# Kernel optimization log

Hardware: AMD Instinct MI355X
Metric: run time of the kernel (lower is better)

Reference implementation:

```python
import jax, jax.numpy as jnp
import numpy as np

B, T, H = 4, 2048, 1024
NH = 16
DK = H // NH  # 64
EPS = 1e-12


def setup_inputs() -> dict:
    key = jax.random.key(0)
    ks = jax.random.split(key, 20)
    s = 0.02
    inp = {
        "hidden_states": jax.random.normal(ks[0], (B, T, H), jnp.float32),
        "source_states": jax.random.normal(ks[1], (B, T, H), jnp.float32),
        "source_len": jax.random.randint(ks[2], (B,), 0, T, jnp.int64),
        # attention params (Linear: y = x @ W + b)
        "Wq": s * jax.random.normal(ks[3], (H, H), jnp.float32),
        "bq": jnp.zeros((H,), jnp.float32),
        "Wk": s * jax.random.normal(ks[4], (H, H), jnp.float32),
        "bk": jnp.zeros((H,), jnp.float32),
        "Wv": s * jax.random.normal(ks[5], (H, H), jnp.float32),
        "bv": jnp.zeros((H,), jnp.float32),
        "Wd": s * jax.random.normal(ks[6], (H, H), jnp.float32),
        "bd": jnp.zeros((H,), jnp.float32),
        # Fp: Linear -> ReLU -> (dropout, eval=id) -> Linear -> (dropout)
        "Wp1": s * jax.random.normal(ks[7], (H, H), jnp.float32),
        "bp1": jnp.zeros((H,), jnp.float32),
        "Wp2": s * jax.random.normal(ks[8], (H, H), jnp.float32),
        "bp2": jnp.zeros((H,), jnp.float32),
        # LayerNorm
        "ln_g": jnp.ones((H,), jnp.float32),
        "ln_b": jnp.zeros((H,), jnp.float32),
    }
    return inp


def _split_heads(x):
    # (B, T, H) -> (B, NH, T, DK)
    return x.reshape(B, T, NH, DK).transpose(0, 2, 1, 3)


def reference(hidden_states, source_states, source_len, Wq, bq, Wk, bk, Wv, bv,
              Wd, bd, Wp1, bp1, Wp2, bp2, ln_g, ln_b):
    # P = Fp(source_states), masked to valid source positions
    P = jax.nn.relu(source_states @ Wp1 + bp1) @ Wp2 + bp2  # (B,T,H)
    rng = jnp.arange(T)[None, :]                              # (1,T)
    source_mask = rng < source_len[:, None]                   # (B,T) bool
    P = P * source_mask[:, :, None].astype(P.dtype)

    q = _split_heads(hidden_states @ Wq + bq)  # (B,NH,T,DK)
    k = _split_heads(P @ Wk + bk)
    v = _split_heads(P @ Wv + bv)

    scores = jnp.einsum('bhqd,bhkd->bhqk', q, k) / jnp.sqrt(jnp.float32(DK))
    scores = scores + (1.0 - source_mask[:, None, None, :].astype(scores.dtype)) * -10000.0
    probs = jax.nn.softmax(scores.astype(jnp.float32), axis=-1).astype(hidden_states.dtype)

    ctx = jnp.einsum('bhqk,bhkd->bhqd', probs, v)            # (B,NH,T,DK)
    ctx = ctx.transpose(0, 2, 1, 3).reshape(B, T, H)

    attn_out = ctx @ Wd + bd
    x = attn_out + hidden_states
    mu = jnp.mean(x, axis=-1, keepdims=True)
    var = jnp.mean(jnp.square(x - mu), axis=-1, keepdims=True)
    out = (x - mu) * jax.lax.rsqrt(var + EPS) * ln_g + ln_b
    return out
```

## Files before the change

kernel.cpp:

```cpp
#include <hip/hip_runtime.h>
#include <hip/hip_bf16.h>

#define BB 4
#define TT 2048
#define HH 1024
#define NHH 16
#define DKK 64

typedef __attribute__((ext_vector_type(8))) short bf16x8;
typedef __attribute__((ext_vector_type(4))) float f32x4;

__device__ __forceinline__ unsigned short f2bf(float f) {
    union { float f; unsigned u; } v; v.f = f;
    unsigned r = v.u + 0x7fffu + ((v.u >> 16) & 1u);
    return (unsigned short)(r >> 16);
}

__device__ __forceinline__ void gload_lds16(const unsigned short* g, unsigned short* l) {
    __builtin_amdgcn_global_load_lds(
        (const __attribute__((address_space(1))) unsigned int*)g,
        (__attribute__((address_space(3))) unsigned int*)l, 16, 0, 0);
}

__global__ __launch_bounds__(256) void cvt2_kernel(const float* __restrict__ in0,
                                                   const float* __restrict__ in1,
                                                   unsigned short* __restrict__ out0,
                                                   unsigned short* __restrict__ out1, int n4) {
    const float* in = blockIdx.y ? in1 : in0;
    unsigned short* out = blockIdx.y ? out1 : out0;
    int i = blockIdx.x * blockDim.x + threadIdx.x;
    if (i < n4) {
        float4 v = reinterpret_cast<const float4*>(in)[i];
        union { unsigned short u[4]; unsigned long long ll; } o;
        o.u[0] = f2bf(v.x); o.u[1] = f2bf(v.y); o.u[2] = f2bf(v.z); o.u[3] = f2bf(v.w);
        reinterpret_cast<unsigned long long*>(out)[i] = o.ll;
    }
}

__global__ __launch_bounds__(256) void wtcvt6_kernel(
    const float* __restrict__ W0, const float* __restrict__ W1, const float* __restrict__ W2,
    const float* __restrict__ W3, const float* __restrict__ W4, const float* __restrict__ W5,
    unsigned short* __restrict__ T0, unsigned short* __restrict__ T1, unsigned short* __restrict__ T2,
    unsigned short* __restrict__ T3, unsigned short* __restrict__ T4, unsigned short* __restrict__ T5) {
    const float* W; unsigned short* Wt;
    switch (blockIdx.z) {
        case 0: W = W0; Wt = T0; break;
        case 1: W = W1; Wt = T1; break;
        case 2: W = W2; Wt = T2; break;
        case 3: W = W3; Wt = T3; break;
        case 4: W = W4; Wt = T4; break;
        default: W = W5; Wt = T5; break;
    }
    __shared__ float t[32][33];
    int bx = blockIdx.x * 32, by = blockIdx.y * 32;
    int tx = threadIdx.x, ty = threadIdx.y;
#pragma unroll
    for (int i = 0; i < 32; i += 8)
        t[ty + i][tx] = W[(size_t)(by + ty + i) * HH + bx + tx];
    __syncthreads();
#pragma unroll
    for (int i = 0; i < 32; i += 8)
        Wt[(size_t)(bx + ty + i) * HH + by + tx] = f2bf(t[tx][ty + i]);
}

template <int EPI, bool SKIP>
__global__ __launch_bounds__(256) void gemm_kernel(
    const unsigned short* __restrict__ A, const unsigned short* __restrict__ Bt,
    const float* __restrict__ bias, unsigned short* __restrict__ Cb,
    float* __restrict__ Cf, const float* __restrict__ resid,
    const int* __restrict__ slen, int M, int N, int K) {
    __shared__ unsigned short As[128 * 64];
    __shared__ unsigned short Bs[128 * 64];
    int flat = blockIdx.y * 8 + blockIdx.x;
    int xcd = flat & 7, idx = flat >> 3;
    int bx = (idx & 7) * 128;
    int by = (xcd + ((idx >> 3) << 3)) * 128;
    if constexpr (SKIP) {
        int slb = slen[by >> 11];
        int ktend = ((slb + 63) >> 6) << 6;
        if (ktend == 0) ktend = 64;
        if ((by & (TT - 1)) >= ktend) return;
    }
    int tid = threadIdx.x, lane = tid & 63, w = tid >> 6;
    int wr = (w >> 1) * 64, wc = (w & 1) * 64;

    f32x4 acc[4][4] = {};
    for (int k0 = 0; k0 < K; k0 += 64) {
        __syncthreads();
#pragma unroll
        for (int c = 0; c < 4; c++) {
            int idx2 = c * 256 + tid;
            int r = idx2 >> 3, col = (idx2 & 7) * 8;
            gload_lds16(&A[(size_t)(by + r) * K + k0 + col], &As[idx2 * 8]);
            gload_lds16(&Bt[(size_t)(bx + r) * K + k0 + col], &Bs[idx2 * 8]);
        }
        __syncthreads();
#pragma unroll
        for (int kk = 0; kk < 2; kk++) {
            bf16x8 a[4], b[4];
#pragma unroll
            for (int i = 0; i < 4; i++)
                a[i] = *(bf16x8*)&As[(wr + i * 16 + (lane & 15)) * 64 + kk * 32 + (lane >> 4) * 8];
#pragma unroll
            for (int j = 0; j < 4; j++)
                b[j] = *(bf16x8*)&Bs[(wc + j * 16 + (lane & 15)) * 64 + kk * 32 + (lane >> 4) * 8];
#pragma unroll
            for (int i = 0; i < 4; i++)
#pragma unroll
                for (int j = 0; j < 4; j++)
                    acc[i][j] = __builtin_amdgcn_mfma_f32_16x16x32_bf16(a[i], b[j], acc[i][j], 0, 0, 0);
        }
    }

    int sl = 0;
    if constexpr (EPI == 2) sl = slen[by >> 11];
#pragma unroll
    for (int i = 0; i < 4; i++)
#pragma unroll
        for (int j = 0; j < 4; j++)
#pragma unroll
            for (int r = 0; r < 4; r++) {
                int row = by + wr + i * 16 + (lane >> 4) * 4 + r;
                int col = bx + wc + j * 16 + (lane & 15);
                float v = acc[i][j][r] + bias[col];
                if constexpr (EPI == 1) v = fmaxf(v, 0.f);
                if constexpr (EPI == 2) { int t = row & (TT - 1); if (t >= sl) v = 0.f; }
                if constexpr (EPI == 6) v *= 0.18033688f;
                if constexpr (EPI == 1 || EPI == 2) {
                    Cb[(size_t)row * N + col] = f2bf(v);
                } else if constexpr (EPI == 3 || EPI == 6) {
                    int b = row >> 11, t = row & (TT - 1), h = col >> 6, d = col & 63;
                    Cb[((size_t)((b * NHH + h) * TT + t)) * DKK + d] = f2bf(v);
                } else if constexpr (EPI == 4) {
                    int b = row >> 11, t = row & (TT - 1), h = col >> 6, d = col & 63;
                    Cb[((size_t)((b * NHH + h) * DKK + d)) * TT + t] = f2bf(v);
                } else if constexpr (EPI == 5) {
                    Cf[(size_t)row * N + col] = v + resid[(size_t)row * N + col];
                }
            }
}

__global__ __launch_bounds__(512) void attn_kernel(
    const unsigned short* __restrict__ Q, const unsigned short* __restrict__ K,
    const unsigned short* __restrict__ Vt, const int* __restrict__ slen,
    unsigned short* __restrict__ ctx) {
    __shared__ unsigned short Ks[2][64 * 64];
    __shared__ unsigned short Vs[2][64 * 64];
    __shared__ unsigned short Pl[8][16 * 64];
    int tid = threadIdx.x, lane = tid & 63, w = tid >> 6;
    int c = lane & 15, g = lane >> 4;
    int b = blockIdx.z, h = blockIdx.y, q0 = blockIdx.x * 128;
    size_t bh = (size_t)(b * NHH + h);
    int sl = slen[b];
    int ktend = ((sl + 63) >> 6) << 6;
    if (ktend == 0) ktend = 64;

    bf16x8 qf[2];
    int qrow = q0 + w * 16 + c;
#pragma unroll
    for (int half = 0; half < 2; half++)
        qf[half] = *(const bf16x8*)&Q[(bh * TT + qrow) * DKK + half * 32 + g * 8];

    char* Pw = (char*)&Pl[w][0];
    unsigned swz = (unsigned)((c & 7) << 4);

    int sr = tid >> 3, ss = tid & 7;
    int scol = (ss ^ (sr & 7)) * 8;

    gload_lds16(&K[(bh * TT + sr) * DKK + scol], &Ks[0][tid * 8]);
    gload_lds16(&Vt[(bh * DKK + sr) * TT + scol], &Vs[0][tid * 8]);
    int cur = 0;

    float m_ = -INFINITY, l_ = 0.f;
    f32x4 o[4] = {};

    for (int kt = 0; kt < ktend; kt += 64) {
        __syncthreads();
        if (kt + 64 < ktend) {
            gload_lds16(&K[(bh * TT + kt + 64 + sr) * DKK + scol], &Ks[cur ^ 1][tid * 8]);
            gload_lds16(&Vt[(bh * DKK + sr) * TT + kt + 64 + scol], &Vs[cur ^ 1][tid * 8]);
        }

        f32x4 s[4] = {};
        __builtin_amdgcn_s_setprio(1);
#pragma unroll
        for (int j = 0; j < 4; j++)
#pragma unroll
            for (int half = 0; half < 2; half++) {
                bf16x8 kf = *(bf16x8*)((char*)&Ks[cur][0] + (j * 16 + c) * 128 +
                                       (((unsigned)(half * 64 + g * 16)) ^ swz));
                s[j] = __builtin_amdgcn_mfma_f32_16x16x32_bf16(kf, qf[half], s[j], 0, 0, 0);
            }
        __builtin_amdgcn_s_setprio(0);

        if (kt + 64 > sl) {
#pragma unroll
            for (int j = 0; j < 4; j++) {
                int kbase = kt + j * 16 + g * 4;
#pragma unroll
                for (int r = 0; r < 4; r++)
                    if (kbase + r >= sl) s[j][r] = -14427.0f;
            }
        }

        float tmax = -INFINITY;
#pragma unroll
        for (int j = 0; j < 4; j++)
#pragma unroll
            for (int r = 0; r < 4; r++) tmax = fmaxf(tmax, s[j][r]);
        tmax = fmaxf(tmax, __shfl_xor(tmax, 16));
        tmax = fmaxf(tmax, __shfl_xor(tmax, 32));

        float p[4][4];
        float ps = 0.f;
        if (__all(tmax <= m_ + 8.f)) {
#pragma unroll
            for (int j = 0; j < 4; j++)
#pragma unroll
                for (int r = 0; r < 4; r++) {
                    p[j][r] = __builtin_amdgcn_exp2f(s[j][r] - m_);
                    ps += p[j][r];
                }
            ps += __shfl_xor(ps, 16);
            ps += __shfl_xor(ps, 32);
            l_ += ps;
        } else {
            float mn = fmaxf(m_, tmax);
            float alpha = __builtin_amdgcn_exp2f(m_ - mn);
#pragma unroll
            for (int j = 0; j < 4; j++)
#pragma unroll
                for (int r = 0; r < 4; r++) {
                    p[j][r] = __builtin_amdgcn_exp2f(s[j][r] - mn);
                    ps += p[j][r];
                }
            ps += __shfl_xor(ps, 16);
            ps += __shfl_xor(ps, 32);
            l_ = l_ * alpha + ps;
            m_ = mn;
            float av[4];
#pragma unroll
            for (int r = 0; r < 4; r++) av[r] = __shfl(alpha, g * 4 + r);
#pragma unroll
            for (int go = 0; go < 4; go++)
#pragma unroll
                for (int r = 0; r < 4; r++) o[go][r] *= av[r];
        }

#pragma unroll
        for (int j = 0; j < 4; j++) {
            __hip_bfloat162 lo = __float22bfloat162_rn(make_float2(p[j][0], p[j][1]));
            __hip_bfloat162 hi = __float22bfloat162_rn(make_float2(p[j][2], p[j][3]));
            uint2 u;
            u.x = *(unsigned*)&lo;
            u.y = *(unsigned*)&hi;
            *(uint2*)(Pw + c * 128 + (((unsigned)(j * 32 + g * 8)) ^ swz)) = u;
        }
        bf16x8 pf0 = *(bf16x8*)(Pw + c * 128 + (((unsigned)(g * 16)) ^ swz));
        bf16x8 pf1 = *(bf16x8*)(Pw + c * 128 + (((unsigned)(64 + g * 16)) ^ swz));

        __builtin_amdgcn_s_setprio(1);
#pragma unroll
        for (int go = 0; go < 4; go++) {
            bf16x8 vf0 = *(bf16x8*)((char*)&Vs[cur][0] + (go * 16 + c) * 128 +
                                    (((unsigned)(g * 16)) ^ swz));
            o[go] = __builtin_amdgcn_mfma_f32_16x16x32_bf16(pf0, vf0, o[go], 0, 0, 0);
            bf16x8 vf1 = *(bf16x8*)((char*)&Vs[cur][0] + (go * 16 + c) * 128 +
                                    (((unsigned)(64 + g * 16)) ^ swz));
            o[go] = __builtin_amdgcn_mfma_f32_16x16x32_bf16(pf1, vf1, o[go], 0, 0, 0);
        }
        __builtin_amdgcn_s_setprio(0);
        cur ^= 1;
    }

    float linv[4];
#pragma unroll
    for (int r = 0; r < 4; r++) linv[r] = 1.f / __shfl(l_, g * 4 + r);
#pragma unroll
    for (int go = 0; go < 4; go++)
#pragma unroll
        for (int r = 0; r < 4; r++) {
            int t = q0 + w * 16 + g * 4 + r;
            int col = h * DKK + go * 16 + c;
            ctx[((size_t)(b * TT + t)) * HH + col] = f2bf(o[go][r] * linv[r]);
        }
}

__global__ __launch_bounds__(256) void ln_kernel(float* __restrict__ x,
                                                 const float* __restrict__ gam,
                                                 const float* __restrict__ bet) {
    int row = blockIdx.x, tid = threadIdx.x;
    float4 v = reinterpret_cast<float4*>(x)[(size_t)row * 256 + tid];
    float s = v.x + v.y + v.z + v.w;
#pragma unroll
    for (int m = 1; m < 64; m <<= 1) s += __shfl_xor(s, m);
    __shared__ float red[4], red2[4];
    if ((tid & 63) == 0) red[tid >> 6] = s;
    __syncthreads();
    float mean = (red[0] + red[1] + red[2] + red[3]) * (1.f / 1024.f);
    float dx0 = v.x - mean, dx1 = v.y - mean, dx2 = v.z - mean, dx3 = v.w - mean;
    float ss = dx0 * dx0 + dx1 * dx1 + dx2 * dx2 + dx3 * dx3;
#pragma unroll
    for (int m = 1; m < 64; m <<= 1) ss += __shfl_xor(ss, m);
    if ((tid & 63) == 0) red2[tid >> 6] = ss;
    __syncthreads();
    float var = (red2[0] + red2[1] + red2[2] + red2[3]) * (1.f / 1024.f);
    float rs = rsqrtf(var + 1e-12f);
    int c = tid * 4;
    float4 ov;
    ov.x = dx0 * rs * gam[c + 0] + bet[c + 0];
    ov.y = dx1 * rs * gam[c + 1] + bet[c + 1];
    ov.z = dx2 * rs * gam[c + 2] + bet[c + 2];
    ov.w = dx3 * rs * gam[c + 3] + bet[c + 3];
    reinterpret_cast<float4*>(x)[(size_t)row * 256 + tid] = ov;
}

extern "C" void kernel_launch(void* const* d_in, const int* in_sizes, int n_in,
                              void* d_out, int out_size, void* d_ws, size_t ws_size,
                              hipStream_t stream) {
    const float* hid  = (const float*)d_in[0];
    const float* src  = (const float*)d_in[1];
    const int* slen   = (const int*)d_in[2];
    const float* Wq  = (const float*)d_in[3];  const float* bq  = (const float*)d_in[4];
    const float* Wk  = (const float*)d_in[5];  const float* bk  = (const float*)d_in[6];
    const float* Wv  = (const float*)d_in[7];  const float* bv  = (const float*)d_in[8];
    const float* Wd  = (const float*)d_in[9];  const float* bd  = (const float*)d_in[10];
    const float* Wp1 = (const float*)d_in[11]; const float* bp1 = (const float*)d_in[12];
    const float* Wp2 = (const float*)d_in[13]; const float* bp2 = (const float*)d_in[14];
    const float* lng = (const float*)d_in[15]; const float* lnb = (const float*)d_in[16];

    char* ws = (char*)d_ws;
    const size_t MB = 1ull << 20;
    unsigned short* Wqt  = (unsigned short*)(ws + 0 * MB);
    unsigned short* Wkt  = (unsigned short*)(ws + 2 * MB);
    unsigned short* Wvt  = (unsigned short*)(ws + 4 * MB);
    unsigned short* Wdt  = (unsigned short*)(ws + 6 * MB);
    unsigned short* Wp1t = (unsigned short*)(ws + 8 * MB);
    unsigned short* Wp2t = (unsigned short*)(ws + 10 * MB);
    unsigned short* hidb = (unsigned short*)(ws + 12 * MB);
    unsigned short* srcb = (unsigned short*)(ws + 28 * MB);
    unsigned short* Ptmp = (unsigned short*)(ws + 44 * MB);
    unsigned short* Pb   = (unsigned short*)(ws + 60 * MB);
    unsigned short* Qb   = (unsigned short*)(ws + 76 * MB);
    unsigned short* Kb   = hidb;
    unsigned short* Vtb  = Ptmp;
    unsigned short* ctxb = srcb;

    wtcvt6_kernel<<<dim3(32, 32, 6), dim3(32, 8), 0, stream>>>(
        Wq, Wk, Wv, Wd, Wp1, Wp2, Wqt, Wkt, Wvt, Wdt, Wp1t, Wp2t);

    const int n4 = (BB * TT * HH) / 4;
    cvt2_kernel<<<dim3(n4 / 256, 2), 256, 0, stream>>>(hid, src, hidb, srcb, n4);

    dim3 gg(8, 64);
    gemm_kernel<1, true><<<gg, 256, 0, stream>>>(srcb, Wp1t, bp1, Ptmp, nullptr, nullptr, slen, BB * TT, HH, HH);
    gemm_kernel<2, true><<<gg, 256, 0, stream>>>(Ptmp, Wp2t, bp2, Pb, nullptr, nullptr, slen, BB * TT, HH, HH);
    gemm_kernel<6, false><<<gg, 256, 0, stream>>>(hidb, Wqt, bq, Qb, nullptr, nullptr, slen, BB * TT, HH, HH);
    gemm_kernel<3, true><<<gg, 256, 0, stream>>>(Pb, Wkt, bk, Kb, nullptr, nullptr, slen, BB * TT, HH, HH);
    gemm_kernel<4, true><<<gg, 256, 0, stream>>>(Pb, Wvt, bv, Vtb, nullptr, nullptr, slen, BB * TT, HH, HH);
    attn_kernel<<<dim3(TT / 128, NHH, BB), 512, 0, stream>>>(Qb, Kb, Vtb, slen, ctxb);
    gemm_kernel<5, false><<<gg, 256, 0, stream>>>(ctxb, Wdt, bd, nullptr, (float*)d_out, hid, slen, BB * TT, HH, HH);
    ln_kernel<<<BB * TT, 256, 0, stream>>>((float*)d_out, lng, lnb);
}
```

Before: 269.5 us.

## Use 128-wide KV tiles in attention, drop double-buffering, flatten grid

The attention kernel now processes 128 keys per iteration with a single LDS buffer loaded synchronously (two barriers), instead of 64-key tiles with asynchronous double-buffered prefetch. The softmax exponentials and bf16 packing are merged into one loop, and P·V is done in two 64-key halves. The grid is flattened so consecutive blocks cover different batch-heads for the same query tile, changing the scheduling order. This halves the loop iterations and barriers but gives up load/compute overlap and raises register use with 8 score accumulators.

Result: slower. 282.7 us (+4.9%).

```diff
diff --git a/kernel.cpp b/kernel.cpp
--- a/kernel.cpp
+++ b/kernel.cpp
@@ -144,13 +144,16 @@
     const unsigned short* __restrict__ Q, const unsigned short* __restrict__ K,
     const unsigned short* __restrict__ Vt, const int* __restrict__ slen,
     unsigned short* __restrict__ ctx) {
-    __shared__ unsigned short Ks[2][64 * 64];
-    __shared__ unsigned short Vs[2][64 * 64];
+    __shared__ unsigned short Ks[128 * 64];
+    __shared__ unsigned short Vs[64 * 128];
     __shared__ unsigned short Pl[8][16 * 64];
     int tid = threadIdx.x, lane = tid & 63, w = tid >> 6;
     int c = lane & 15, g = lane >> 4;
-    int b = blockIdx.z, h = blockIdx.y, q0 = blockIdx.x * 128;
-    size_t bh = (size_t)(b * NHH + h);
+    int flat = blockIdx.x;
+    int bh = flat & 63;
+    int q0 = (flat >> 6) * 128;
+    int b = bh >> 4;
+    size_t bhs = (size_t)bh;
     int sl = slen[b];
     int ktend = ((sl + 63) >> 6) << 6;
     if (ktend == 0) ktend = 64;
@@ -159,43 +162,41 @@
     int qrow = q0 + w * 16 + c;
 #pragma unroll
     for (int half = 0; half < 2; half++)
-        qf[half] = *(const bf16x8*)&Q[(bh * TT + qrow) * DKK + half * 32 + g * 8];
+        qf[half] = *(const bf16x8*)&Q[(bhs * TT + qrow) * DKK + half * 32 + g * 8];
 
     char* Pw = (char*)&Pl[w][0];
     unsigned swz = (unsigned)((c & 7) << 4);
 
-    int sr = tid >> 3, ss = tid & 7;
-    int scol = (ss ^ (sr & 7)) * 8;
-
-    gload_lds16(&K[(bh * TT + sr) * DKK + scol], &Ks[0][tid * 8]);
-    gload_lds16(&Vt[(bh * DKK + sr) * TT + scol], &Vs[0][tid * 8]);
-    int cur = 0;
-
     float m_ = -INFINITY, l_ = 0.f;
     f32x4 o[4] = {};
 
-    for (int kt = 0; kt < ktend; kt += 64) {
+    for (int kt = 0; kt < ktend; kt += 128) {
         __syncthreads();
-        if (kt + 64 < ktend) {
-            gload_lds16(&K[(bh * TT + kt + 64 + sr) * DKK + scol], &Ks[cur ^ 1][tid * 8]);
-            gload_lds16(&Vt[(bh * DKK + sr) * TT + kt + 64 + scol], &Vs[cur ^ 1][tid * 8]);
-        }
-
-        f32x4 s[4] = {};
+#pragma unroll
+        for (int cc = 0; cc < 2; cc++) {
+            int idx2 = tid + cc * 512;
+            int kr = idx2 >> 3, ks = idx2 & 7;
+            gload_lds16(&K[(bhs * TT + kt + kr) * DKK + ((ks ^ (kr & 7)) * 8)], &Ks[idx2 * 8]);
+            int vr = idx2 >> 4, vs = idx2 & 15;
+            gload_lds16(&Vt[(bhs * DKK + vr) * TT + kt + ((vs ^ (vr & 7)) * 8)], &Vs[idx2 * 8]);
+        }
+        __syncthreads();
+
+        f32x4 s[8] = {};
         __builtin_amdgcn_s_setprio(1);
 #pragma unroll
-        for (int j = 0; j < 4; j++)
+        for (int j = 0; j < 8; j++)
 #pragma unroll
             for (int half = 0; half < 2; half++) {
-                bf16x8 kf = *(bf16x8*)((char*)&Ks[cur][0] + (j * 16 + c) * 128 +
+                bf16x8 kf = *(bf16x8*)((char*)Ks + (j * 16 + c) * 128 +
                                        (((unsigned)(half * 64 + g * 16)) ^ swz));
                 s[j] = __builtin_amdgcn_mfma_f32_16x16x32_bf16(kf, qf[half], s[j], 0, 0, 0);
             }
         __builtin_amdgcn_s_setprio(0);
 
-        if (kt + 64 > sl) {
-#pragma unroll
-            for (int j = 0; j < 4; j++) {
+        if (kt + 128 > sl) {
+#pragma unroll
+            for (int j = 0; j < 8; j++) {
                 int kbase = kt + j * 16 + g * 4;
 #pragma unroll
                 for (int r = 0; r < 4; r++)
@@ -205,37 +206,34 @@
 
         float tmax = -INFINITY;
 #pragma unroll
-        for (int j = 0; j < 4; j++)
+        for (int j = 0; j < 8; j++)
 #pragma unroll
             for (int r = 0; r < 4; r++) tmax = fmaxf(tmax, s[j][r]);
         tmax = fmaxf(tmax, __shfl_xor(tmax, 16));
         tmax = fmaxf(tmax, __shfl_xor(tmax, 32));
 
-        float p[4][4];
+        uint2 pu[8];
         float ps = 0.f;
-        if (__all(tmax <= m_ + 8.f)) {
-#pragma unroll
-            for (int j = 0; j < 4; j++)
-#pragma unroll
-                for (int r = 0; r < 4; r++) {
-                    p[j][r] = __builtin_amdgcn_exp2f(s[j][r] - m_);
-                    ps += p[j][r];
-                }
-            ps += __shfl_xor(ps, 16);
-            ps += __shfl_xor(ps, 32);
+        bool defer = __all(tmax <= m_ + 8.f);
+        float mn = defer ? m_ : fmaxf(m_, tmax);
+#pragma unroll
+        for (int j = 0; j < 8; j++) {
+            float p0 = __builtin_amdgcn_exp2f(s[j][0] - mn);
+            float p1 = __builtin_amdgcn_exp2f(s[j][1] - mn);
+            float p2 = __builtin_amdgcn_exp2f(s[j][2] - mn);
+            float p3 = __builtin_amdgcn_exp2f(s[j][3] - mn);
+            ps += (p0 + p1) + (p2 + p3);
+            __hip_bfloat162 lo = __float22bfloat162_rn(make_float2(p0, p1));
+            __hip_bfloat162 hi = __float22bfloat162_rn(make_float2(p2, p3));
+            pu[j].x = *(unsigned*)&lo;
+            pu[j].y = *(unsigned*)&hi;
+        }
+        ps += __shfl_xor(ps, 16);
+        ps += __shfl_xor(ps, 32);
+        if (defer) {
             l_ += ps;
         } else {
-            float mn = fmaxf(m_, tmax);
             float alpha = __builtin_amdgcn_exp2f(m_ - mn);
-#pragma unroll
-            for (int j = 0; j < 4; j++)
-#pragma unroll
-                for (int r = 0; r < 4; r++) {
-                    p[j][r] = __builtin_amdgcn_exp2f(s[j][r] - mn);
-                    ps += p[j][r];
-                }
-            ps += __shfl_xor(ps, 16);
-            ps += __shfl_xor(ps, 32);
             l_ = l_ * alpha + ps;
             m_ = mn;
             float av[4];
@@ -248,29 +246,24 @@
         }
 
 #pragma unroll
-        for (int j = 0; j < 4; j++) {
-            __hip_bfloat162 lo = __float22bfloat162_rn(make_float2(p[j][0], p[j][1]));
-            __hip_bfloat162 hi = __float22bfloat162_rn(make_float2(p[j][2], p[j][3]));
-            uint2 u;
-            u.x = *(unsigned*)&lo;
-            u.y = *(unsigned*)&hi;
-            *(uint2*)(Pw + c * 128 + (((unsigned)(j * 32 + g * 8)) ^ swz)) = u;
-        }
-        bf16x8 pf0 = *(bf16x8*)(Pw + c * 128 + (((unsigned)(g * 16)) ^ swz));
-        bf16x8 pf1 = *(bf16x8*)(Pw + c * 128 + (((unsigned)(64 + g * 16)) ^ swz));
-
-        __builtin_amdgcn_s_setprio(1);
-#pragma unroll
-        for (int go = 0; go < 4; go++) {
-            bf16x8 vf0 = *(bf16x8*)((char*)&Vs[cur][0] + (go * 16 + c) * 128 +
-                                    (((unsigned)(g * 16)) ^ swz));
-            o[go] = __builtin_amdgcn_mfma_f32_16x16x32_bf16(pf0, vf0, o[go], 0, 0, 0);
-            bf16x8 vf1 = *(bf16x8*)((char*)&Vs[cur][0] + (go * 16 + c) * 128 +
-                                    (((unsigned)(64 + g * 16)) ^ swz));
-            o[go] = __builtin_amdgcn_mfma_f32_16x16x32_bf16(pf1, vf1, o[go], 0, 0, 0);
-        }
-        __builtin_amdgcn_s_setprio(0);
-        cur ^= 1;
+        for (int hb = 0; hb < 2; hb++) {
+#pragma unroll
+            for (int j2 = 0; j2 < 4; j2++)
+                *(uint2*)(Pw + c * 128 + (((unsigned)(j2 * 32 + g * 8)) ^ swz)) = pu[hb * 4 + j2];
+            bf16x8 pf0 = *(bf16x8*)(Pw + c * 128 + (((unsigned)(g * 16)) ^ swz));
+            bf16x8 pf1 = *(bf16x8*)(Pw + c * 128 + (((unsigned)(64 + g * 16)) ^ swz));
+            __builtin_amdgcn_s_setprio(1);
+#pragma unroll
+            for (int go = 0; go < 4; go++) {
+                bf16x8 vf0 = *(bf16x8*)((char*)Vs + (go * 16 + c) * 256 +
+                                        (((unsigned)(hb * 128 + g * 16)) ^ swz));
+                o[go] = __builtin_amdgcn_mfma_f32_16x16x32_bf16(pf0, vf0, o[go], 0, 0, 0);
+                bf16x8 vf1 = *(bf16x8*)((char*)Vs + (go * 16 + c) * 256 +
+                                        (((unsigned)(hb * 128 + 64 + g * 16)) ^ swz));
+                o[go] = __builtin_amdgcn_mfma_f32_16x16x32_bf16(pf1, vf1, o[go], 0, 0, 0);
+            }
+            __builtin_amdgcn_s_setprio(0);
+        }
     }
 
     float linv[4];
@@ -281,7 +274,7 @@
 #pragma unroll
         for (int r = 0; r < 4; r++) {
             int t = q0 + w * 16 + g * 4 + r;
-            int col = h * DKK + go * 16 + c;
+            int col = (bh & 15) * DKK + go * 16 + c;
             ctx[((size_t)(b * TT + t)) * HH + col] = f2bf(o[go][r] * linv[r]);
         }
 }
@@ -358,7 +351,7 @@
     gemm_kernel<6, false><<<gg, 256, 0, stream>>>(hidb, Wqt, bq, Qb, nullptr, nullptr, slen, BB * TT, HH, HH);
     gemm_kernel<3, true><<<gg, 256, 0, stream>>>(Pb, Wkt, bk, Kb, nullptr, nullptr, slen, BB * TT, HH, HH);
     gemm_kernel<4, true><<<gg, 256, 0, stream>>>(Pb, Wvt, bv, Vtb, nullptr, nullptr, slen, BB * TT, HH, HH);
-    attn_kernel<<<dim3(TT / 128, NHH, BB), 512, 0, stream>>>(Qb, Kb, Vtb, slen, ctxb);
+    attn_kernel<<<dim3(64 * (TT / 128)), 512, 0, stream>>>(Qb, Kb, Vtb, slen, ctxb);
     gemm_kernel<5, false><<<gg, 256, 0, stream>>>(ctxb, Wdt, bd, nullptr, (float*)d_out, hid, slen, BB * TT, HH, HH);
     ln_kernel<<<BB * TT, 256, 0, stream>>>((float*)d_out, lng, lnb);
 }
```

## Load attention K/V fragments directly from global memory and flatten the grid

Applied to the files above, without the earlier changes.

The attention kernel drops its double-buffered LDS staging of K and V tiles and the per-iteration __syncthreads, and each wave reads its MFMA operand fragments straight from global memory instead, relying on L1/L2 to serve the reuse across the 8 waves. The grid becomes 1D with batch-head as the fastest index, so blocks sharing the same query tile but different heads launch together and same-K/V blocks spread out. The softmax branch is merged so the exp loop is shared between the deferred and rescale paths. The aim is to remove barrier and LDS traffic, at the cost of redundant global/cache loads per wave and no explicit prefetch overlap.

New measurement: 530.8 us. +97.0%, slower.

```diff
diff --git a/kernel.cpp b/kernel.cpp
--- a/kernel.cpp
+++ b/kernel.cpp
@@ -144,13 +144,14 @@
     const unsigned short* __restrict__ Q, const unsigned short* __restrict__ K,
     const unsigned short* __restrict__ Vt, const int* __restrict__ slen,
     unsigned short* __restrict__ ctx) {
-    __shared__ unsigned short Ks[2][64 * 64];
-    __shared__ unsigned short Vs[2][64 * 64];
     __shared__ unsigned short Pl[8][16 * 64];
     int tid = threadIdx.x, lane = tid & 63, w = tid >> 6;
     int c = lane & 15, g = lane >> 4;
-    int b = blockIdx.z, h = blockIdx.y, q0 = blockIdx.x * 128;
-    size_t bh = (size_t)(b * NHH + h);
+    int flat = blockIdx.x;
+    int bh = flat & 63;
+    int q0 = (flat >> 6) * 128;
+    int b = bh >> 4;
+    size_t bhs = (size_t)bh;
     int sl = slen[b];
     int ktend = ((sl + 63) >> 6) << 6;
     if (ktend == 0) ktend = 64;
@@ -159,38 +160,28 @@
     int qrow = q0 + w * 16 + c;
 #pragma unroll
     for (int half = 0; half < 2; half++)
-        qf[half] = *(const bf16x8*)&Q[(bh * TT + qrow) * DKK + half * 32 + g * 8];
+        qf[half] = *(const bf16x8*)&Q[(bhs * TT + qrow) * DKK + half * 32 + g * 8];
 
     char* Pw = (char*)&Pl[w][0];
     unsigned swz = (unsigned)((c & 7) << 4);
 
-    int sr = tid >> 3, ss = tid & 7;
-    int scol = (ss ^ (sr & 7)) * 8;
-
-    gload_lds16(&K[(bh * TT + sr) * DKK + scol], &Ks[0][tid * 8]);
-    gload_lds16(&Vt[(bh * DKK + sr) * TT + scol], &Vs[0][tid * 8]);
-    int cur = 0;
+    const unsigned short* Kbase = &K[(bhs * TT + c) * DKK + g * 8];
+    const unsigned short* Vbase = &Vt[(bhs * DKK + c) * TT + g * 8];
 
     float m_ = -INFINITY, l_ = 0.f;
     f32x4 o[4] = {};
 
     for (int kt = 0; kt < ktend; kt += 64) {
-        __syncthreads();
-        if (kt + 64 < ktend) {
-            gload_lds16(&K[(bh * TT + kt + 64 + sr) * DKK + scol], &Ks[cur ^ 1][tid * 8]);
-            gload_lds16(&Vt[(bh * DKK + sr) * TT + kt + 64 + scol], &Vs[cur ^ 1][tid * 8]);
-        }
-
         f32x4 s[4] = {};
         __builtin_amdgcn_s_setprio(1);
 #pragma unroll
-        for (int j = 0; j < 4; j++)
-#pragma unroll
-            for (int half = 0; half < 2; half++) {
-                bf16x8 kf = *(bf16x8*)((char*)&Ks[cur][0] + (j * 16 + c) * 128 +
-                                       (((unsigned)(half * 64 + g * 16)) ^ swz));
-                s[j] = __builtin_amdgcn_mfma_f32_16x16x32_bf16(kf, qf[half], s[j], 0, 0, 0);
-            }
+        for (int j = 0; j < 4; j++) {
+            const unsigned short* kr = Kbase + (size_t)(kt + j * 16) * DKK;
+            bf16x8 kf0 = *(const bf16x8*)kr;
+            s[j] = __builtin_amdgcn_mfma_f32_16x16x32_bf16(kf0, qf[0], s[j], 0, 0, 0);
+            bf16x8 kf1 = *(const bf16x8*)(kr + 32);
+            s[j] = __builtin_amdgcn_mfma_f32_16x16x32_bf16(kf1, qf[1], s[j], 0, 0, 0);
+        }
         __builtin_amdgcn_s_setprio(0);
 
         if (kt + 64 > sl) {
@@ -213,29 +204,21 @@
 
         float p[4][4];
         float ps = 0.f;
-        if (__all(tmax <= m_ + 8.f)) {
-#pragma unroll
-            for (int j = 0; j < 4; j++)
-#pragma unroll
-                for (int r = 0; r < 4; r++) {
-                    p[j][r] = __builtin_amdgcn_exp2f(s[j][r] - m_);
-                    ps += p[j][r];
-                }
-            ps += __shfl_xor(ps, 16);
-            ps += __shfl_xor(ps, 32);
+        bool defer = __all(tmax <= m_ + 8.f);
+        float mn = defer ? m_ : fmaxf(m_, tmax);
+#pragma unroll
+        for (int j = 0; j < 4; j++)
+#pragma unroll
+            for (int r = 0; r < 4; r++) {
+                p[j][r] = __builtin_amdgcn_exp2f(s[j][r] - mn);
+                ps += p[j][r];
+            }
+        ps += __shfl_xor(ps, 16);
+        ps += __shfl_xor(ps, 32);
+        if (defer) {
             l_ += ps;
         } else {
-            float mn = fmaxf(m_, tmax);
             float alpha = __builtin_amdgcn_exp2f(m_ - mn);
-#pragma unroll
-            for (int j = 0; j < 4; j++)
-#pragma unroll
-                for (int r = 0; r < 4; r++) {
-                    p[j][r] = __builtin_amdgcn_exp2f(s[j][r] - mn);
-                    ps += p[j][r];
-                }
-            ps += __shfl_xor(ps, 16);
-            ps += __shfl_xor(ps, 32);
             l_ = l_ * alpha + ps;
             m_ = mn;
             float av[4];
@@ -262,15 +245,13 @@
         __builtin_amdgcn_s_setprio(1);
 #pragma unroll
         for (int go = 0; go < 4; go++) {
-            bf16x8 vf0 = *(bf16x8*)((char*)&Vs[cur][0] + (go * 16 + c) * 128 +
-                                    (((unsigned)(g * 16)) ^ swz));
+            const unsigned short* vr = Vbase + (size_t)(go * 16) * TT + kt;
+            bf16x8 vf0 = *(const bf16x8*)vr;
             o[go] = __builtin_amdgcn_mfma_f32_16x16x32_bf16(pf0, vf0, o[go], 0, 0, 0);
-            bf16x8 vf1 = *(bf16x8*)((char*)&Vs[cur][0] + (go * 16 + c) * 128 +
-                                    (((unsigned)(64 + g * 16)) ^ swz));
+            bf16x8 vf1 = *(const bf16x8*)(vr + 32);
             o[go] = __builtin_amdgcn_mfma_f32_16x16x32_bf16(pf1, vf1, o[go], 0, 0, 0);
         }
         __builtin_amdgcn_s_setprio(0);
-        cur ^= 1;
     }
 
     float linv[4];
@@ -281,7 +262,7 @@
 #pragma unroll
         for (int r = 0; r < 4; r++) {
             int t = q0 + w * 16 + g * 4 + r;
-            int col = h * DKK + go * 16 + c;
+            int col = (bh & 15) * DKK + go * 16 + c;
             ctx[((size_t)(b * TT + t)) * HH + col] = f2bf(o[go][r] * linv[r]);
         }
 }
@@ -358,7 +339,7 @@
     gemm_kernel<6, false><<<gg, 256, 0, stream>>>(hidb, Wqt, bq, Qb, nullptr, nullptr, slen, BB * TT, HH, HH);
     gemm_kernel<3, true><<<gg, 256, 0, stream>>>(Pb, Wkt, bk, Kb, nullptr, nullptr, slen, BB * TT, HH, HH);
     gemm_kernel<4, true><<<gg, 256, 0, stream>>>(Pb, Wvt, bv, Vtb, nullptr, nullptr, slen, BB * TT, HH, HH);
-    attn_kernel<<<dim3(TT / 128, NHH, BB), 512, 0, stream>>>(Qb, Kb, Vtb, slen, ctxb);
+    attn_kernel<<<dim3(64 * (TT / 128)), 512, 0, stream>>>(Qb, Kb, Vtb, slen, ctxb);
     gemm_kernel<5, false><<<gg, 256, 0, stream>>>(ctxb, Wdt, bd, nullptr, (float*)d_out, hid, slen, BB * TT, HH, HH);
     ln_kernel<<<BB * TT, 256, 0, stream>>>((float*)d_out, lng, lnb);
 }
```
